# Performance work log

Hardware: AMD Instinct MI355X
Metric: run time of the kernel (lower is better)

## Reference

```python
import math
import jax, jax.numpy as jnp
import numpy as np

N_HEADS = 32
N_KV_HEADS = 8
HEAD_DIM = 128
DIM = 4096
B = 32
MAX_SEQ = 4096
Q_LEN = 1
START_POS = 4095


def setup_inputs() -> dict:
    key = jax.random.key(0)
    ks = jax.random.split(key, 9)
    x = jax.random.normal(ks[0], (B, Q_LEN, DIM), dtype=jnp.float32)
    # RoPE angles for the current positions (seqlen=Q_LEN, half head_dim pairs)
    inv_freq = 1.0 / (500000.0 ** (np.arange(0, HEAD_DIM, 2, dtype=np.float32) / HEAD_DIM))
    pos = np.arange(START_POS, START_POS + Q_LEN, dtype=np.float32)
    ang = pos[:, None] * inv_freq[None, :]  # [Q_LEN, HEAD_DIM//2]
    freqs_cos = jnp.asarray(np.cos(ang), dtype=jnp.float32)
    freqs_sin = jnp.asarray(np.sin(ang), dtype=jnp.float32)
    cache_k = jax.random.normal(ks[1], (B, MAX_SEQ, N_KV_HEADS, HEAD_DIM), dtype=jnp.float32)
    cache_v = jax.random.normal(ks[2], (B, MAX_SEQ, N_KV_HEADS, HEAD_DIM), dtype=jnp.float32)
    s = 0.02
    wq = jax.random.normal(ks[3], (N_HEADS * HEAD_DIM, DIM), dtype=jnp.float32) * s
    wk = jax.random.normal(ks[4], (N_KV_HEADS * HEAD_DIM, DIM), dtype=jnp.float32) * s
    wv = jax.random.normal(ks[5], (N_KV_HEADS * HEAD_DIM, DIM), dtype=jnp.float32) * s
    wo = jax.random.normal(ks[6], (DIM, N_HEADS * HEAD_DIM), dtype=jnp.float32) * s
    return {"x": x, "start_pos": START_POS, "freqs_cos": freqs_cos, "freqs_sin": freqs_sin,
            "cache_k": cache_k, "cache_v": cache_v, "wq": wq, "wk": wk, "wv": wv, "wo": wo}


def _rope(t, cos, sin):
    # t: [B, S, h, hd]; cos/sin: [S, hd//2]; complex multiply on (even, odd) pairs
    tr = t.reshape(*t.shape[:-1], HEAD_DIM // 2, 2)
    a, b = tr[..., 0], tr[..., 1]
    c = cos[None, :, None, :]
    s = sin[None, :, None, :]
    out = jnp.stack([a * c - b * s, a * s + b * c], axis=-1)
    return out.reshape(t.shape)


def reference(x, start_pos, freqs_cos, freqs_sin, cache_k, cache_v, wq, wk, wv, wo):
    bsz, seqlen, _ = x.shape
    n_rep = N_HEADS // N_KV_HEADS
    xq = jnp.einsum('bsd,od->bso', x, wq).reshape(bsz, seqlen, N_HEADS, HEAD_DIM)
    xk = jnp.einsum('bsd,od->bso', x, wk).reshape(bsz, seqlen, N_KV_HEADS, HEAD_DIM)
    xv = jnp.einsum('bsd,od->bso', x, wv).reshape(bsz, seqlen, N_KV_HEADS, HEAD_DIM)
    xq = _rope(xq, freqs_cos, freqs_sin)
    xk = _rope(xk, freqs_cos, freqs_sin)
    # KV-cache update (start_pos is a static Python int)
    cache_k = cache_k.at[:, start_pos:start_pos + seqlen].set(xk)
    cache_v = cache_v.at[:, start_pos:start_pos + seqlen].set(xv)
    keys = cache_k[:, :start_pos + seqlen]    # [B, T, Hkv, hd]
    values = cache_v[:, :start_pos + seqlen]  # [B, T, Hkv, hd]
    # GQA: group query heads [H] -> [Hkv, n_rep]; avoids materializing repeated KV
    q = xq.reshape(bsz, seqlen, N_KV_HEADS, n_rep, HEAD_DIM)
    scale = 1.0 / math.sqrt(HEAD_DIM)
    scores = jnp.einsum('bsgrd,btgd->bgrst', q, keys) * scale  # [B, Hkv, n_rep, S, T]
    probs = jax.nn.softmax(scores, axis=-1)
    out = jnp.einsum('bgrst,btgd->bsgrd', probs, values)
    out = out.reshape(bsz, seqlen, N_HEADS * HEAD_DIM)
    return jnp.einsum('bse,de->bsd', out, wo)
```

## Files before the change

### kernel.cpp

```cpp
#include <hip/hip_runtime.h>

#define B_    32
#define DIM_  4096
#define NH_   32
#define NKV_  8
#define HD_   128
#define TSEQ  4096
#define NQKV  6144
#define GSPLIT 16
#define BK    32
#define NT    256
#define TSPL  4
#define TS    1024

__device__ __forceinline__ const float* wrow(const float* w0, const float* w1,
                                             const float* w2, int b1, int b2, int col) {
    if (col < b1) return w0 + (size_t)col * DIM_;
    if (col < b2) return w1 + (size_t)(col - b1) * DIM_;
    return w2 + (size_t)(col - b2) * DIM_;
}

__global__ __launch_bounds__(128) void gemm32(
    const float* __restrict__ A, const float* __restrict__ w0,
    const float* __restrict__ w1, const float* __restrict__ w2,
    int b1, int b2, int N, float* __restrict__ po)
{
    __shared__ __align__(16) float wt[BK][NT + 4];
    __shared__ __align__(16) float xs[BK][36];
    const int tid = threadIdx.x;
    const int cg  = tid & 31;
    const int bg  = tid >> 5;
    const int ct  = blockIdx.x * NT;
    const int k0  = blockIdx.y * (DIM_ / GSPLIT);

    float acc[8][8];
    #pragma unroll
    for (int i = 0; i < 8; ++i)
        #pragma unroll
        for (int j = 0; j < 8; ++j) acc[i][j] = 0.f;

    const int kq = (tid & 7) * 4;
    const int rr = tid >> 3;

    for (int kt = 0; kt < DIM_ / GSPLIT; kt += BK) {
        const int kb = k0 + kt;
        #pragma unroll
        for (int st = 0; st < 16; ++st) {
            const int c = st * 16 + rr;
            const float* wr = wrow(w0, w1, w2, b1, b2, ct + c);
            const float4 wv = *(const float4*)(wr + kb + kq);
            wt[kq + 0][c] = wv.x; wt[kq + 1][c] = wv.y;
            wt[kq + 2][c] = wv.z; wt[kq + 3][c] = wv.w;
        }
        #pragma unroll
        for (int st = 0; st < 2; ++st) {
            const int b = st * 16 + rr;
            const float4 xv = *(const float4*)(A + (size_t)b * DIM_ + kb + kq);
            xs[kq + 0][b] = xv.x; xs[kq + 1][b] = xv.y;
            xs[kq + 2][b] = xv.z; xs[kq + 3][b] = xv.w;
        }
        __syncthreads();
        #pragma unroll 8
        for (int kk = 0; kk < BK; ++kk) {
            const float4 xa = *(const float4*)&xs[kk][bg * 8];
            const float4 xb = *(const float4*)&xs[kk][bg * 8 + 4];
            const float4 wa = *(const float4*)&wt[kk][cg * 4];
            const float4 wb = *(const float4*)&wt[kk][128 + cg * 4];
            const float xv[8] = {xa.x, xa.y, xa.z, xa.w, xb.x, xb.y, xb.z, xb.w};
            const float wv[8] = {wa.x, wa.y, wa.z, wa.w, wb.x, wb.y, wb.z, wb.w};
            #pragma unroll
            for (int i = 0; i < 8; ++i)
                #pragma unroll
                for (int j = 0; j < 8; ++j)
                    acc[i][j] = fmaf(xv[i], wv[j], acc[i][j]);
        }
        __syncthreads();
    }
    const size_t srow = (size_t)blockIdx.y * B_;
    #pragma unroll
    for (int i = 0; i < 8; ++i) {
        const int b = bg * 8 + i;
        const float4 o0 = make_float4(acc[i][0], acc[i][1], acc[i][2], acc[i][3]);
        const float4 o1 = make_float4(acc[i][4], acc[i][5], acc[i][6], acc[i][7]);
        *(float4*)&po[(srow + b) * N + ct + cg * 4]       = o0;
        *(float4*)&po[(srow + b) * N + ct + 128 + cg * 4] = o1;
    }
}

__global__ void reduce_rope(const float* __restrict__ po,
                            const float* __restrict__ fc, const float* __restrict__ fs,
                            float* __restrict__ qkv)
{
    const int pid = blockIdx.x * 256 + threadIdx.x;
    const int b  = pid / 3072;
    const int c0 = (pid - b * 3072) * 2;
    float v0 = 0.f, v1 = 0.f;
    #pragma unroll
    for (int s = 0; s < GSPLIT; ++s) {
        const float* p = po + ((size_t)s * B_ + b) * NQKV + c0;
        v0 += p[0]; v1 += p[1];
    }
    if (c0 < DIM_ + NKV_ * HD_) {
        const int i = (c0 & 127) >> 1;
        const float c = fc[i], sn = fs[i];
        const float o0 = v0 * c - v1 * sn;
        const float o1 = v0 * sn + v1 * c;
        v0 = o0; v1 = o1;
    }
    qkv[(size_t)b * NQKV + c0]     = v0;
    qkv[(size_t)b * NQKV + c0 + 1] = v1;
}

__global__ __launch_bounds__(256) void attn_partial(
    const float* __restrict__ qkv, const float* __restrict__ ck,
    const float* __restrict__ cv,
    float* __restrict__ po , float* __restrict__ pl )
{
    const int blk = blockIdx.x;
    const int s = blk & 3;
    const int g = (blk >> 2) & 7;
    const int b = blk >> 5;
    const int tid    = threadIdx.x;
    const int copy   = tid >> 5;
    const int lane32 = tid & 31;
    const int d4     = lane32 * 4;
    const float* qb = qkv + (size_t)b * NQKV;

    const float4 q0 = *(const float4*)(qb + (g * 4 + 0) * HD_ + d4);
    const float4 q1 = *(const float4*)(qb + (g * 4 + 1) * HD_ + d4);
    const float4 q2 = *(const float4*)(qb + (g * 4 + 2) * HD_ + d4);
    const float4 q3 = *(const float4*)(qb + (g * 4 + 3) * HD_ + d4);

    float acc[4][4] = {{0.f}};
    float l0 = 0.f, l1 = 0.f, l2 = 0.f, l3 = 0.f;
    const float scale = 0.08838834764831845f;
    const int t0 = s * TS + copy;

    for (int it = 0; it < TS / 8; ++it) {
        const int t = t0 + it * 8;
        const float *kp, *vp;
        if (t == TSEQ - 1) {
            kp = qb + DIM_ + g * HD_;
            vp = qb + DIM_ + NKV_ * HD_ + g * HD_;
        } else {
            const size_t off = (((size_t)b * TSEQ + t) * NKV_ + g) * HD_;
            kp = ck + off; vp = cv + off;
        }
        const float4 kv = *(const float4*)(kp + d4);
        float p0 = kv.x*q0.x + kv.y*q0.y + kv.z*q0.z + kv.w*q0.w;
        float p1 = kv.x*q1.x + kv.y*q1.y + kv.z*q1.z + kv.w*q1.w;
        float p2 = kv.x*q2.x + kv.y*q2.y + kv.z*q2.z + kv.w*q2.w;
        float p3 = kv.x*q3.x + kv.y*q3.y + kv.z*q3.z + kv.w*q3.w;
        #pragma unroll
        for (int off = 1; off < 32; off <<= 1) {
            p0 += __shfl_xor(p0, off);
            p1 += __shfl_xor(p1, off);
            p2 += __shfl_xor(p2, off);
            p3 += __shfl_xor(p3, off);
        }
        p0 = __expf(p0 * scale); p1 = __expf(p1 * scale);
        p2 = __expf(p2 * scale); p3 = __expf(p3 * scale);
        l0 += p0; l1 += p1; l2 += p2; l3 += p3;
        const float4 vv = *(const float4*)(vp + d4);
        acc[0][0] += p0*vv.x; acc[0][1] += p0*vv.y; acc[0][2] += p0*vv.z; acc[0][3] += p0*vv.w;
        acc[1][0] += p1*vv.x; acc[1][1] += p1*vv.y; acc[1][2] += p1*vv.z; acc[1][3] += p1*vv.w;
        acc[2][0] += p2*vv.x; acc[2][1] += p2*vv.y; acc[2][2] += p2*vv.z; acc[2][3] += p2*vv.w;
        acc[3][0] += p3*vv.x; acc[3][1] += p3*vv.y; acc[3][2] += p3*vv.z; acc[3][3] += p3*vv.w;
    }

    __shared__ __align__(16) float ob[8][4][HD_];
    __shared__ float lb[8][4];
    #pragma unroll
    for (int r = 0; r < 4; ++r) {
        ob[copy][r][d4+0] = acc[r][0]; ob[copy][r][d4+1] = acc[r][1];
        ob[copy][r][d4+2] = acc[r][2]; ob[copy][r][d4+3] = acc[r][3];
    }
    if (lane32 == 0) { lb[copy][0] = l0; lb[copy][1] = l1; lb[copy][2] = l2; lb[copy][3] = l3; }
    __syncthreads();
    #pragma unroll
    for (int e = tid; e < 512; e += 256) {
        float sum = 0.f;
        #pragma unroll
        for (int c = 0; c < 8; ++c) sum += ob[c][e >> 7][e & 127];
        po[(size_t)blk * 512 + e] = sum;
    }
    if (tid < 4) {
        float sum = 0.f;
        #pragma unroll
        for (int c = 0; c < 8; ++c) sum += lb[c][tid];
        pl[blk * 4 + tid] = sum;
    }
}

__global__ void attn_combine(const float* __restrict__ po, const float* __restrict__ pl,
                             float* __restrict__ ao)
{
    const int bg  = blockIdx.x;
    const int tid = threadIdx.x;
    const int e0  = tid * 4;
    const int r   = e0 >> 7;
    float4 o = make_float4(0.f, 0.f, 0.f, 0.f);
    float ls = 0.f;
    #pragma unroll
    for (int s = 0; s < TSPL; ++s) {
        const float4 v = *(const float4*)&po[((size_t)bg * TSPL + s) * 512 + e0];
        o.x += v.x; o.y += v.y; o.z += v.z; o.w += v.w;
        ls += pl[(bg * TSPL + s) * 4 + r];
    }
    const float inv = 1.f / ls;
    o.x *= inv; o.y *= inv; o.z *= inv; o.w *= inv;
    const int b = bg >> 3, g = bg & 7;
    *(float4*)&ao[(size_t)b * DIM_ + g * 512 + e0] = o;
}

__global__ void reduce_out(const float* __restrict__ po, float* __restrict__ out)
{
    const int i = blockIdx.x * 256 + threadIdx.x;
    const int b = i >> 12, c = i & 4095;
    float v = 0.f;
    #pragma unroll
    for (int s = 0; s < GSPLIT; ++s) v += po[((size_t)s * B_ + b) * DIM_ + c];
    out[i] = v;
}

extern "C" void kernel_launch(void* const* d_in, const int* in_sizes, int n_in,
                              void* d_out, int out_size, void* d_ws, size_t ws_size,
                              hipStream_t stream)
{
    (void)in_sizes; (void)n_in; (void)out_size; (void)ws_size;
    const float* x  = (const float*)d_in[0];
    const float* fc = (const float*)d_in[2];
    const float* fs = (const float*)d_in[3];
    const float* ck = (const float*)d_in[4];
    const float* cv = (const float*)d_in[5];
    const float* wq = (const float*)d_in[6];
    const float* wk = (const float*)d_in[7];
    const float* wv = (const float*)d_in[8];
    const float* wo = (const float*)d_in[9];
    float* out = (float*)d_out;
    float* ws  = (float*)d_ws;

    float* qkv  = ws;
    float* aout = ws + 196608;
    float* apo  = ws + 327680;
    float* apl  = ws + 851968;
    float* gp   = ws + 856064;

    gemm32<<<dim3(NQKV / NT, GSPLIT), 128, 0, stream>>>(
        x, wq, wk, wv, DIM_, DIM_ + NKV_ * HD_, NQKV, gp);
    reduce_rope<<<dim3((B_ * (NQKV / 2)) / 256), 256, 0, stream>>>(gp, fc, fs, qkv);
    attn_partial<<<dim3(B_ * NKV_ * TSPL), 256, 0, stream>>>(qkv, ck, cv, apo, apl);
    attn_combine<<<dim3(B_ * NKV_), 128, 0, stream>>>(apo, apl, aout);
    gemm32<<<dim3(DIM_ / NT, GSPLIT), 128, 0, stream>>>(
        aout, wo, wo, wo, DIM_, DIM_, DIM_, gp);
    reduce_out<<<dim3((B_ * DIM_) / 256), 256, 0, stream>>>(gp, out);
}
```

Baseline: 286.6 us.

## Double attention and GEMM split-K parallelism, use 16-lane groups per key

Doubles the split-K factor of the projection GEMMs and the number of sequence splits in decode attention, so more blocks are launched. Inside attention, each key row is now handled by 16 lanes with 8 elements each instead of 32 lanes with 4. That gives more tokens in flight per block and a shorter shuffle reduction, followed by a cross-group shuffle reduce before the shared-memory combine. Workspace offsets are moved to fit the larger partial buffers. The cost is more partial sums to reduce and higher register pressure.

```diff
diff --git a/kernel.cpp b/kernel.cpp
--- a/kernel.cpp
+++ b/kernel.cpp
@@ -7,11 +7,11 @@
 #define HD_   128
 #define TSEQ  4096
 #define NQKV  6144
-#define GSPLIT 16
+#define GSPLIT 32
 #define BK    32
 #define NT    256
-#define TSPL  4
-#define TS    1024
+#define TSPL  8
+#define TS    512
 
 __device__ __forceinline__ const float* wrow(const float* w0, const float* w1,
                                              const float* w2, int b1, int b2, int col) {
@@ -117,27 +117,35 @@
     float* __restrict__ po , float* __restrict__ pl )
 {
     const int blk = blockIdx.x;
-    const int s = blk & 3;
-    const int g = (blk >> 2) & 7;
-    const int b = blk >> 5;
+    const int s = blk & (TSPL - 1);
+    const int g = (blk / TSPL) & 7;
+    const int b = blk / (TSPL * NKV_);
     const int tid    = threadIdx.x;
-    const int copy   = tid >> 5;
-    const int lane32 = tid & 31;
-    const int d4     = lane32 * 4;
+    const int grp    = tid >> 4;
+    const int lane16 = tid & 15;
+    const int wv     = tid >> 6;
+    const int g4     = (tid >> 4) & 3;
+    const int d8     = lane16 * 8;
     const float* qb = qkv + (size_t)b * NQKV;
 
-    const float4 q0 = *(const float4*)(qb + (g * 4 + 0) * HD_ + d4);
-    const float4 q1 = *(const float4*)(qb + (g * 4 + 1) * HD_ + d4);
-    const float4 q2 = *(const float4*)(qb + (g * 4 + 2) * HD_ + d4);
-    const float4 q3 = *(const float4*)(qb + (g * 4 + 3) * HD_ + d4);
-
-    float acc[4][4] = {{0.f}};
-    float l0 = 0.f, l1 = 0.f, l2 = 0.f, l3 = 0.f;
+    float4 qa[4], qc[4];
+    #pragma unroll
+    for (int h = 0; h < 4; ++h) {
+        qa[h] = *(const float4*)(qb + (g * 4 + h) * HD_ + d8);
+        qc[h] = *(const float4*)(qb + (g * 4 + h) * HD_ + d8 + 4);
+    }
+
+    float acc[4][8];
+    #pragma unroll
+    for (int h = 0; h < 4; ++h)
+        #pragma unroll
+        for (int e = 0; e < 8; ++e) acc[h][e] = 0.f;
+    float l[4] = {0.f, 0.f, 0.f, 0.f};
     const float scale = 0.08838834764831845f;
-    const int t0 = s * TS + copy;
-
-    for (int it = 0; it < TS / 8; ++it) {
-        const int t = t0 + it * 8;
+    const int t0 = s * TS + grp;
+
+    for (int it = 0; it < TS / 16; ++it) {
+        const int t = t0 + it * 16;
         const float *kp, *vp;
         if (t == TSEQ - 1) {
             kp = qb + DIM_ + g * HD_;
@@ -146,48 +154,69 @@
             const size_t off = (((size_t)b * TSEQ + t) * NKV_ + g) * HD_;
             kp = ck + off; vp = cv + off;
         }
-        const float4 kv = *(const float4*)(kp + d4);
-        float p0 = kv.x*q0.x + kv.y*q0.y + kv.z*q0.z + kv.w*q0.w;
-        float p1 = kv.x*q1.x + kv.y*q1.y + kv.z*q1.z + kv.w*q1.w;
-        float p2 = kv.x*q2.x + kv.y*q2.y + kv.z*q2.z + kv.w*q2.w;
-        float p3 = kv.x*q3.x + kv.y*q3.y + kv.z*q3.z + kv.w*q3.w;
-        #pragma unroll
-        for (int off = 1; off < 32; off <<= 1) {
-            p0 += __shfl_xor(p0, off);
-            p1 += __shfl_xor(p1, off);
-            p2 += __shfl_xor(p2, off);
-            p3 += __shfl_xor(p3, off);
-        }
-        p0 = __expf(p0 * scale); p1 = __expf(p1 * scale);
-        p2 = __expf(p2 * scale); p3 = __expf(p3 * scale);
-        l0 += p0; l1 += p1; l2 += p2; l3 += p3;
-        const float4 vv = *(const float4*)(vp + d4);
-        acc[0][0] += p0*vv.x; acc[0][1] += p0*vv.y; acc[0][2] += p0*vv.z; acc[0][3] += p0*vv.w;
-        acc[1][0] += p1*vv.x; acc[1][1] += p1*vv.y; acc[1][2] += p1*vv.z; acc[1][3] += p1*vv.w;
-        acc[2][0] += p2*vv.x; acc[2][1] += p2*vv.y; acc[2][2] += p2*vv.z; acc[2][3] += p2*vv.w;
-        acc[3][0] += p3*vv.x; acc[3][1] += p3*vv.y; acc[3][2] += p3*vv.z; acc[3][3] += p3*vv.w;
-    }
-
-    __shared__ __align__(16) float ob[8][4][HD_];
-    __shared__ float lb[8][4];
-    #pragma unroll
-    for (int r = 0; r < 4; ++r) {
-        ob[copy][r][d4+0] = acc[r][0]; ob[copy][r][d4+1] = acc[r][1];
-        ob[copy][r][d4+2] = acc[r][2]; ob[copy][r][d4+3] = acc[r][3];
-    }
-    if (lane32 == 0) { lb[copy][0] = l0; lb[copy][1] = l1; lb[copy][2] = l2; lb[copy][3] = l3; }
+        const float4 k0 = *(const float4*)(kp + d8);
+        const float4 k1 = *(const float4*)(kp + d8 + 4);
+        float p[4];
+        #pragma unroll
+        for (int h = 0; h < 4; ++h) {
+            p[h] = k0.x*qa[h].x + k0.y*qa[h].y + k0.z*qa[h].z + k0.w*qa[h].w
+                 + k1.x*qc[h].x + k1.y*qc[h].y + k1.z*qc[h].z + k1.w*qc[h].w;
+        }
+        #pragma unroll
+        for (int off = 1; off < 16; off <<= 1) {
+            #pragma unroll
+            for (int h = 0; h < 4; ++h) p[h] += __shfl_xor(p[h], off);
+        }
+        #pragma unroll
+        for (int h = 0; h < 4; ++h) {
+            p[h] = __expf(p[h] * scale);
+            l[h] += p[h];
+        }
+        const float4 v0 = *(const float4*)(vp + d8);
+        const float4 v1 = *(const float4*)(vp + d8 + 4);
+        #pragma unroll
+        for (int h = 0; h < 4; ++h) {
+            acc[h][0] += p[h]*v0.x; acc[h][1] += p[h]*v0.y;
+            acc[h][2] += p[h]*v0.z; acc[h][3] += p[h]*v0.w;
+            acc[h][4] += p[h]*v1.x; acc[h][5] += p[h]*v1.y;
+            acc[h][6] += p[h]*v1.z; acc[h][7] += p[h]*v1.w;
+        }
+    }
+
+    #pragma unroll
+    for (int off = 16; off < 64; off <<= 1) {
+        #pragma unroll
+        for (int h = 0; h < 4; ++h) {
+            #pragma unroll
+            for (int e = 0; e < 8; ++e) acc[h][e] += __shfl_xor(acc[h][e], off);
+            l[h] += __shfl_xor(l[h], off);
+        }
+    }
+
+    __shared__ __align__(16) float ob[4][4][HD_];
+    __shared__ float lb[4][4];
+    if (g4 == 0) {
+        #pragma unroll
+        for (int h = 0; h < 4; ++h)
+            #pragma unroll
+            for (int e = 0; e < 8; ++e) ob[wv][h][d8 + e] = acc[h][e];
+        if (lane16 == 0) {
+            #pragma unroll
+            for (int h = 0; h < 4; ++h) lb[wv][h] = l[h];
+        }
+    }
     __syncthreads();
     #pragma unroll
     for (int e = tid; e < 512; e += 256) {
         float sum = 0.f;
         #pragma unroll
-        for (int c = 0; c < 8; ++c) sum += ob[c][e >> 7][e & 127];
+        for (int c = 0; c < 4; ++c) sum += ob[c][e >> 7][e & 127];
         po[(size_t)blk * 512 + e] = sum;
     }
     if (tid < 4) {
         float sum = 0.f;
         #pragma unroll
-        for (int c = 0; c < 8; ++c) sum += lb[c][tid];
+        for (int c = 0; c < 4; ++c) sum += lb[c][tid];
         pl[blk * 4 + tid] = sum;
     }
 }
@@ -243,8 +272,8 @@
     float* qkv  = ws;
     float* aout = ws + 196608;
     float* apo  = ws + 327680;
-    float* apl  = ws + 851968;
-    float* gp   = ws + 856064;
+    float* apl  = ws + 1376256;
+    float* gp   = ws + 1384448;
 
     gemm32<<<dim3(NQKV / NT, GSPLIT), 128, 0, stream>>>(
         x, wq, wk, wv, DIM_, DIM_ + NKV_ * HD_, NQKV, gp);
```

Result: no change. 285.3 us (-0.5%).
